# Optimization experiments

Measured on AMD Instinct MI355X. Metric: run time of the kernel, lower is better.

Reference implementation:

```python
import jax, jax.numpy as jnp
import numpy as np
from jax import lax

B, L, C_IN = 64, 2000, 4
F, K, PAD = 256, 13, 6
POOL = 4
H, DH = 8, 64
DM, NCLS = 100, 2
NOUT = L // POOL  # 500


def _rel_dist_bias():
    # RelativePosition: |clip(k - q, +-(L-1))| / (L-1), then MaxPool2d(k=POOL)
    r = jnp.arange(L)
    d = jnp.abs(jnp.clip(r[None, :] - r[:, None], -(L - 1), L - 1)).astype(jnp.float32) / (L - 1)
    d = d.reshape(NOUT, POOL, NOUT, POOL).max(axis=(1, 3))  # [NOUT, NOUT]
    return d


def setup_inputs() -> dict:
    key = jax.random.key(0)
    ks = jax.random.split(key, 8)
    s = lambda fan: 1.0 / np.sqrt(fan)
    return {
        "x": jax.random.normal(ks[0], (B, L, C_IN), jnp.float32),
        "conv_w": jax.random.normal(ks[1], (F, C_IN, K), jnp.float32) * s(C_IN * K),
        "bn_gamma": jnp.ones((F,), jnp.float32),
        "bn_beta": jnp.zeros((F,), jnp.float32),
        "Wq": jax.random.normal(ks[2], (H, F, DH), jnp.float32) * s(F),
        "bq": jnp.zeros((H, DH), jnp.float32),
        "Wk": jax.random.normal(ks[3], (H, F, DH), jnp.float32) * s(F),
        "bk": jnp.zeros((H, DH), jnp.float32),
        "Wv": jax.random.normal(ks[4], (H, F, DH), jnp.float32) * s(F),
        "bv": jnp.zeros((H, DH), jnp.float32),
        "Wm": jax.random.normal(ks[5], (H * DH, DM), jnp.float32) * s(H * DH),
        "bm": jnp.zeros((DM,), jnp.float32),
        "Wo": jax.random.normal(ks[6], (DM, NCLS), jnp.float32) * s(DM),
        "bo": jnp.zeros((NCLS,), jnp.float32),
    }


def _forward(x, conv_w, bn_gamma, bn_beta, Wq, bq, Wk, bk, Wv, bv, Wm, bm, Wo, bo):
    # CNN frontend: Conv1d (no bias) + BatchNorm (batch stats) + ReLU + MaxPool1d(4)
    xc = jnp.transpose(x, (0, 2, 1))  # [B, C_IN, L]
    y = lax.conv_general_dilated(xc, conv_w, (1,), [(PAD, PAD)],
                                 dimension_numbers=("NCH", "OIH", "NCH"))  # [B, F, L]
    mu = y.mean(axis=(0, 2), keepdims=True)
    var = y.var(axis=(0, 2), keepdims=True)
    y = bn_gamma[None, :, None] * (y - mu) * lax.rsqrt(var + 1e-5) + bn_beta[None, :, None]
    y = jax.nn.relu(y)
    y = y.reshape(B, F, NOUT, POOL).max(axis=-1)  # maxpool k=4
    h = jnp.transpose(y, (0, 2, 1))  # [B, NOUT, F]

    # Per-head Q/K/V projections (stacked over heads)
    q = jnp.einsum("bnf,hfd->bhnd", h, Wq) + bq[None, :, None, :]
    k = jnp.einsum("bnf,hfd->bhnd", h, Wk) + bk[None, :, None, :]
    v = jnp.einsum("bnf,hfd->bhnd", h, Wv) + bv[None, :, None, :]

    scores = jnp.einsum("bhnd,bhmd->bhnm", q, k) / jnp.sqrt(jnp.float32(DH))
    scores = scores - _rel_dist_bias()[None, None]  # relative-position bias
    attn = jax.nn.softmax(scores, axis=-1)
    o = jnp.einsum("bhnm,bhmd->bhnd", attn, v)  # [B, H, NOUT, DH]
    o = jnp.transpose(o, (0, 2, 1, 3)).reshape(B, NOUT, H * DH)

    m = jax.nn.relu(o @ Wm + bm)            # MultiHeadLinear + ReLU
    feat = m.sum(axis=1)                    # readout: sum over positions
    feat = (feat - feat.mean(axis=-1, keepdims=True)) / (feat.std(axis=-1, keepdims=True) + 1e-6)
    return feat @ Wo + bo                   # [B, NCLS]


def reference(x, conv_w, bn_gamma, bn_beta, Wq, bq, Wk, bk, Wv, bv, Wm, bm, Wo, bo):
    return _forward(x, conv_w, bn_gamma, bn_beta, Wq, bq, Wk, bk, Wv, bv, Wm, bm, Wo, bo)
```

## Files before the change

kernel.cpp:

```cpp
#include <hip/hip_runtime.h>
#include <stdint.h>
#include <math.h>

#define NB   64
#define LL   2000
#define CIN  4
#define NF   256
#define KW   13
#define NOUT 500
#define NH   8
#define DH   64
#define DMID 100
#define NCLS 2

#define OFF_PSUM   0
#define OFF_PSQ    16384
#define OFF_SCALE  32768
#define OFF_SHIFT  33024
#define OFF_PART   33280
#define BOFF_WT    337920ull
#define BOFF_WMT   1124352ull
#define BOFF_Q     1239040ull
#define BOFF_K     34007040ull
#define BOFF_VT    66775040ull
#define BOFF_YM    100329472ull
#define BOFF_O     BOFF_YM
#define WS_NEED    133097472ull

__device__ __forceinline__ float blo(uint32_t u) { return __uint_as_float(u << 16); }
__device__ __forceinline__ float bhi(uint32_t u) { return __uint_as_float(u & 0xFFFF0000u); }
__device__ __forceinline__ uint32_t f2bf1(float f) {
  uint32_t x = __float_as_uint(f);
  return (x + 0x7FFFu + ((x >> 16) & 1u)) >> 16;
}
__device__ __forceinline__ uint32_t pack2(float a, float b) {
  return f2bf1(a) | (f2bf1(b) << 16);
}

typedef short bf16x8 __attribute__((ext_vector_type(8)));
typedef float f32x4  __attribute__((ext_vector_type(4)));
union UB { uint4 u; bf16x8 v; };

__device__ __forceinline__ int swz(int row, int colElem) {
  return row * 128 + ((colElem * 2) ^ ((row & 7) << 4));
}

__global__ void k_prep(const float* __restrict__ Wq, const float* __restrict__ Wk,
                       const float* __restrict__ Wv, const float* __restrict__ Wm,
                       uint16_t* __restrict__ WT, uint16_t* __restrict__ WmT) {
  const int g = blockIdx.x;
  if (g < 24) {
    const int which = g >> 3, h = g & 7;
    const float* W = (which == 0 ? Wq : which == 1 ? Wk : Wv) + (size_t)h * NF * DH;
    uint16_t* dst = WT + (size_t)g * DH * NF;
    for (int idx = threadIdx.x; idx < NF * DH; idx += 256) {
      const int f = idx >> 6, d = idx & 63;
      dst[d * NF + f] = (uint16_t)f2bf1(W[idx]);
    }
  } else {
    for (int idx = threadIdx.x; idx < 112 * 512; idx += 256) {
      const int c = idx >> 9, k = idx & 511;
      WmT[idx] = (c < DMID) ? (uint16_t)f2bf1(Wm[k * DMID + c]) : (uint16_t)0;
    }
  }
}

__global__ __launch_bounds__(512) void k_conv(const float* __restrict__ x,
                                              const float* __restrict__ cw,
                                              uint16_t* __restrict__ ymaxT,
                                              float* __restrict__ psum,
                                              float* __restrict__ psq) {
  const int b = blockIdx.x;
  const int fg = blockIdx.y;
  const int tid = threadIdx.x;
  const int n = tid;
  const bool act = (n < NOUT);
  const float* xb = x + (size_t)b * (LL * CIN);

  float4 xw[16];
#pragma unroll
  for (int i = 0; i < 16; ++i) {
    const int p = 4 * n - 6 + i;
    if (act && p >= 0 && p < LL)
      xw[i] = *(const float4*)(xb + (size_t)p * CIN);
    else
      xw[i] = make_float4(0.f, 0.f, 0.f, 0.f);
  }

  __shared__ float redS[8][16];
  __shared__ float redQ[8][16];
  const int wave = tid >> 6, lane = tid & 63;
  uint32_t pw[8];
  float prev = 0.f;

  for (int fi = 0; fi < 16; ++fi) {
    const int f = fg * 16 + fi;
    const float* w = cw + (size_t)f * (CIN * KW);
    float wr[4][13];
#pragma unroll
    for (int c = 0; c < 4; ++c)
#pragma unroll
      for (int k = 0; k < 13; ++k) wr[c][k] = w[c * 13 + k];

    float a0 = 0.f, a1 = 0.f, a2 = 0.f, a3 = 0.f;
#pragma unroll
    for (int k = 0; k < 13; ++k) {
      const float4 p0 = xw[k + 0];
      const float4 p1 = xw[k + 1];
      const float4 p2 = xw[k + 2];
      const float4 p3 = xw[k + 3];
      a0 += wr[0][k] * p0.x + wr[1][k] * p0.y + wr[2][k] * p0.z + wr[3][k] * p0.w;
      a1 += wr[0][k] * p1.x + wr[1][k] * p1.y + wr[2][k] * p1.z + wr[3][k] * p1.w;
      a2 += wr[0][k] * p2.x + wr[1][k] * p2.y + wr[2][k] * p2.z + wr[3][k] * p2.w;
      a3 += wr[0][k] * p3.x + wr[1][k] * p3.y + wr[2][k] * p3.z + wr[3][k] * p3.w;
    }
    const float pm = fmaxf(fmaxf(a0, a1), fmaxf(a2, a3));
    if (fi & 1) pw[fi >> 1] = pack2(prev, pm); else prev = pm;

    float s  = act ? (a0 + a1 + a2 + a3) : 0.f;
    float q2 = act ? (a0 * a0 + a1 * a1 + a2 * a2 + a3 * a3) : 0.f;
#pragma unroll
    for (int off = 32; off >= 1; off >>= 1) {
      s  += __shfl_xor(s,  off, 64);
      q2 += __shfl_xor(q2, off, 64);
    }
    if (lane == 0) { redS[wave][fi] = s; redQ[wave][fi] = q2; }
  }
  if (act) {
    uint16_t* dst = ymaxT + ((size_t)b * NOUT + n) * NF + fg * 16;
    uint4 s0 = make_uint4(pw[0], pw[1], pw[2], pw[3]);
    uint4 s1 = make_uint4(pw[4], pw[5], pw[6], pw[7]);
    *(uint4*)dst = s0;
    *(uint4*)(dst + 8) = s1;
  }
  __syncthreads();
  if (tid < 16) {
    float s = 0.f;
#pragma unroll
    for (int wv = 0; wv < 8; ++wv) s += redS[wv][tid];
    psum[b * NF + fg * 16 + tid] = s;
  } else if (tid < 32) {
    float s = 0.f;
#pragma unroll
    for (int wv = 0; wv < 8; ++wv) s += redQ[wv][tid - 16];
    psq[b * NF + fg * 16 + (tid - 16)] = s;
  }
}

__global__ void k_stats(const float* __restrict__ psum, const float* __restrict__ psq,
                        const float* __restrict__ gamma, const float* __restrict__ beta,
                        float* __restrict__ scale, float* __restrict__ shift) {
  const int f = threadIdx.x;
  float s = 0.f, q = 0.f;
  for (int b = 0; b < NB; ++b) { s += psum[b * NF + f]; q += psq[b * NF + f]; }
  const float inv = 1.0f / (float)(NB * LL);
  const float mean = s * inv;
  const float var = q * inv - mean * mean;
  const float sc = gamma[f] * rsqrtf(var + 1e-5f);
  scale[f] = sc;
  shift[f] = beta[f] - mean * sc;
}

__global__ __launch_bounds__(256, 4) void k_qkv(const uint16_t* __restrict__ ymaxT,
     const float* __restrict__ scale, const float* __restrict__ shift,
     const uint16_t* __restrict__ WT,
     const float* __restrict__ bq, const float* __restrict__ bk, const float* __restrict__ bv,
     uint16_t* __restrict__ qb, uint16_t* __restrict__ kb, uint16_t* __restrict__ vbT) {
  const int g  = blockIdx.x;
  const int nt = blockIdx.y;
  const int b  = blockIdx.z;
  const int which = g >> 3, h = g & 7;
  const int tid = threadIdx.x;
  const int wv = tid >> 6, l = tid & 63;
  const int lg = l >> 4, lq = l & 15;
  const int n0 = nt * 64 + wv * 16;
  const uint16_t* WTg = WT + (size_t)g * DH * NF;
  const float* bias = (which == 0 ? bq : which == 1 ? bk : bv) + h * DH;

  f32x4 acc[4] = {};

  const int an = n0 + lq;
  const uint16_t* abase = ymaxT + ((size_t)b * NOUT + an) * NF;

#pragma unroll
  for (int c = 0; c < 8; ++c) {
    const int f0 = c * 32 + lg * 8;
    const uint4 ar = *(const uint4*)(abase + f0);
    const float4 s0 = *(const float4*)(scale + f0);
    const float4 s1 = *(const float4*)(scale + f0 + 4);
    const float4 h0 = *(const float4*)(shift + f0);
    const float4 h1 = *(const float4*)(shift + f0 + 4);
    UB a;
    a.u.x = pack2(fmaxf(s0.x * blo(ar.x) + h0.x, 0.f), fmaxf(s0.y * bhi(ar.x) + h0.y, 0.f));
    a.u.y = pack2(fmaxf(s0.z * blo(ar.y) + h0.z, 0.f), fmaxf(s0.w * bhi(ar.y) + h0.w, 0.f));
    a.u.z = pack2(fmaxf(s1.x * blo(ar.z) + h1.x, 0.f), fmaxf(s1.y * bhi(ar.z) + h1.y, 0.f));
    a.u.w = pack2(fmaxf(s1.z * blo(ar.w) + h1.z, 0.f), fmaxf(s1.w * bhi(ar.w) + h1.w, 0.f));
#pragma unroll
    for (int t = 0; t < 4; ++t) {
      UB bfr;
      bfr.u = *(const uint4*)(WTg + (size_t)(16 * t + lq) * NF + f0);
      acc[t] = __builtin_amdgcn_mfma_f32_16x16x32_bf16(a.v, bfr.v, acc[t], 0, 0, 0);
    }
  }

  if (which < 2) {
    uint16_t* out = (which == 0 ? qb : kb) + (size_t)(b * NH + h) * NOUT * DH;
#pragma unroll
    for (int t = 0; t < 4; ++t) {
      const int d = 16 * t + lq;
      const float bb = bias[d];
#pragma unroll
      for (int r = 0; r < 4; ++r) {
        const int nn = n0 + 4 * lg + r;
        if (nn < NOUT) out[(size_t)nn * DH + d] = (uint16_t)f2bf1(acc[t][r] + bb);
      }
    }
  } else {
    uint16_t* out = vbT + (size_t)(b * NH + h) * DH * 512;
#pragma unroll
    for (int t = 0; t < 4; ++t) {
      const int d = 16 * t + lq;
      const float bb = bias[d];
#pragma unroll
      for (int r = 0; r < 4; ++r) {
        const int nn = n0 + 4 * lg + r;
        if (nn < NOUT) out[(size_t)d * 512 + nn] = (uint16_t)f2bf1(acc[t][r] + bb);
      }
    }
  }
}

__global__ __launch_bounds__(256, 4) void k_attn(const uint16_t* __restrict__ qb,
                                                 const uint16_t* __restrict__ kb,
                                                 const uint16_t* __restrict__ vbT,
                                                 uint16_t* __restrict__ ob) {
  const int qt = blockIdx.x;
  const int h  = blockIdx.y;
  const int b  = blockIdx.z;
  const int tid = threadIdx.x;
  const int wv = tid >> 6, l = tid & 63;
  const int lg = l >> 4, lq = l & 15;

  __shared__ char smem[24576];
  char* Ks = smem;
  char* Vs = smem + 8192;
  char* Ps = smem + 16384 + wv * 2048;

  const size_t qkbase = (size_t)(b * NH + h) * NOUT * DH;
  const size_t vbase  = (size_t)(b * NH + h) * DH * 512;
  const int q0 = qt * 64 + wv * 16;

  bf16x8 qf[2];
  {
    const int qn = min(q0 + lq, NOUT - 1);
    const uint16_t* src = qb + qkbase + (size_t)qn * DH + lg * 8;
    UB t0, t1;
    t0.u = *(const uint4*)src;
    t1.u = *(const uint4*)(src + 32);
    qf[0] = t0.v; qf[1] = t1.v;
  }

  f32x4 oacc[4] = {};
  float m = -1e30f, lsum = 0.f;
  const int nq = q0 + lq;

  for (int kt = 0; kt < 8; ++kt) {
    const int kv0 = kt * 64;
    __syncthreads();
    {
      const int r = tid >> 2, cc = (tid & 3) * 16;
      const int kn = min(kv0 + r, NOUT - 1);
      const uint16_t* ksrc = kb + qkbase + (size_t)kn * DH + cc;
      uint4 ka = *(const uint4*)ksrc;
      uint4 kb4 = *(const uint4*)(ksrc + 8);
      *(uint4*)(Ks + swz(r, cc))     = ka;
      *(uint4*)(Ks + swz(r, cc + 8)) = kb4;
      const uint16_t* vsrc = vbT + vbase + (size_t)r * 512 + kv0 + cc;
      uint4 va = *(const uint4*)vsrc;
      uint4 vb4 = *(const uint4*)(vsrc + 8);
      *(uint4*)(Vs + swz(r, cc))     = va;
      *(uint4*)(Vs + swz(r, cc + 8)) = vb4;
    }
    __syncthreads();

    f32x4 sacc[4] = {};
#pragma unroll
    for (int c = 0; c < 2; ++c)
#pragma unroll
      for (int s = 0; s < 4; ++s) {
        UB kf;
        kf.u = *(const uint4*)(Ks + swz(16 * s + lq, 32 * c + 8 * lg));
        sacc[s] = __builtin_amdgcn_mfma_f32_16x16x32_bf16(kf.v, qf[c], sacc[s], 0, 0, 0);
      }

    float tmax = -1e30f;
#pragma unroll
    for (int s = 0; s < 4; ++s)
#pragma unroll
      for (int r = 0; r < 4; ++r) {
        const int nk = kv0 + 16 * s + 4 * lg + r;
        float val = sacc[s][r] * 0.125f -
                    (4.0f * fabsf((float)(nq - nk)) + 3.0f) * (1.0f / 1999.0f);
        if (nk >= NOUT) val = -1e30f;
        sacc[s][r] = val;
        tmax = fmaxf(tmax, val);
      }
    tmax = fmaxf(tmax, __shfl_xor(tmax, 16, 64));
    tmax = fmaxf(tmax, __shfl_xor(tmax, 32, 64));
    const float mnew = fmaxf(m, tmax);
    const float corr = __expf(m - mnew);
    m = mnew;
    float ls = 0.f;
#pragma unroll
    for (int s = 0; s < 4; ++s)
#pragma unroll
      for (int r = 0; r < 4; ++r) {
        const float pv = __expf(sacc[s][r] - mnew);
        sacc[s][r] = pv;
        ls += pv;
      }
    ls += __shfl_xor(ls, 16, 64);
    ls += __shfl_xor(ls, 32, 64);
    lsum = lsum * corr + ls;

#pragma unroll
    for (int s = 0; s < 4; ++s) {
      uint2 w;
      w.x = pack2(sacc[s][0], sacc[s][1]);
      w.y = pack2(sacc[s][2], sacc[s][3]);
      *(uint2*)(Ps + swz(lq, 16 * s + 4 * lg)) = w;
    }

    float cr[4];
#pragma unroll
    for (int r = 0; r < 4; ++r) cr[r] = __shfl(corr, 4 * lg + r, 64);
#pragma unroll
    for (int t = 0; t < 4; ++t)
#pragma unroll
      for (int r = 0; r < 4; ++r) oacc[t][r] *= cr[r];

#pragma unroll
    for (int c = 0; c < 2; ++c) {
      UB pf;
      pf.u = *(const uint4*)(Ps + swz(lq, 32 * c + 8 * lg));
#pragma unroll
      for (int t = 0; t < 4; ++t) {
        UB vf;
        vf.u = *(const uint4*)(Vs + swz(16 * t + lq, 32 * c + 8 * lg));
        oacc[t] = __builtin_amdgcn_mfma_f32_16x16x32_bf16(pf.v, vf.v, oacc[t], 0, 0, 0);
      }
    }
  }

  const float inv = 1.0f / lsum;
  float invr[4];
#pragma unroll
  for (int r = 0; r < 4; ++r) invr[r] = __shfl(inv, 4 * lg + r, 64);
#pragma unroll
  for (int t = 0; t < 4; ++t) {
    const int d = 16 * t + lq;
#pragma unroll
    for (int r = 0; r < 4; ++r) {
      const int nn = q0 + 4 * lg + r;
      if (nn < NOUT)
        ob[((size_t)b * NOUT + nn) * (NH * DH) + h * DH + d] =
            (uint16_t)f2bf1(oacc[t][r] * invr[r]);
    }
  }
}

__global__ __launch_bounds__(256, 4) void k_mhl(const uint16_t* __restrict__ ob,
                                                const uint16_t* __restrict__ WmT,
                                                const float* __restrict__ bm,
                                                float* __restrict__ part) {
  const int nt = blockIdx.x;
  const int b  = blockIdx.y;
  const int tid = threadIdx.x;
  const int wv = tid >> 6, l = tid & 63;
  const int lg = l >> 4, lq = l & 15;
  const int n0 = nt * 64 + wv * 16;

  __shared__ float lfeat[4][112];

  f32x4 acc[7] = {};
  const int an = min(n0 + lq, NOUT - 1);
  const uint16_t* abase = ob + ((size_t)b * NOUT + an) * (NH * DH);

  for (int kc = 0; kc < 16; ++kc) {
    const int k0 = kc * 32 + lg * 8;
    UB a;
    a.u = *(const uint4*)(abase + k0);
#pragma unroll
    for (int t = 0; t < 7; ++t) {
      UB bfr;
      bfr.u = *(const uint4*)(WmT + (size_t)(16 * t + lq) * 512 + k0);
      acc[t] = __builtin_amdgcn_mfma_f32_16x16x32_bf16(a.v, bfr.v, acc[t], 0, 0, 0);
    }
  }

#pragma unroll
  for (int t = 0; t < 7; ++t) {
    const int c = 16 * t + lq;
    const float bb = (c < DMID) ? bm[c] : 0.f;
    float s = 0.f;
#pragma unroll
    for (int r = 0; r < 4; ++r) {
      const int nn = n0 + 4 * lg + r;
      if (nn < NOUT) s += fmaxf(acc[t][r] + bb, 0.f);
    }
    s += __shfl_xor(s, 16, 64);
    s += __shfl_xor(s, 32, 64);
    if (lg == 0) lfeat[wv][c] = s;
  }
  __syncthreads();
  if (tid < DMID)
    part[((size_t)b * 8 + nt) * DMID + tid] =
        lfeat[0][tid] + lfeat[1][tid] + lfeat[2][tid] + lfeat[3][tid];
}

__global__ void k_head(const float* __restrict__ part, const float* __restrict__ Wo,
                       const float* __restrict__ bo, float* __restrict__ out) {
  const int b = threadIdx.x;
  float s1 = 0.f;
  for (int c = 0; c < DMID; ++c) {
    float v = 0.f;
    for (int t = 0; t < 8; ++t) v += part[((size_t)b * 8 + t) * DMID + c];
    s1 += v;
  }
  const float mean = s1 / (float)DMID;
  float s2 = 0.f;
  for (int c = 0; c < DMID; ++c) {
    float v = 0.f;
    for (int t = 0; t < 8; ++t) v += part[((size_t)b * 8 + t) * DMID + c];
    const float d = v - mean;
    s2 += d * d;
  }
  const float inv = 1.0f / (sqrtf(s2 / (float)DMID) + 1e-6f);
  float o0 = bo[0], o1 = bo[1];
  for (int c = 0; c < DMID; ++c) {
    float v = 0.f;
    for (int t = 0; t < 8; ++t) v += part[((size_t)b * 8 + t) * DMID + c];
    const float nz = (v - mean) * inv;
    o0 += nz * Wo[c * 2 + 0];
    o1 += nz * Wo[c * 2 + 1];
  }
  out[b * 2 + 0] = o0;
  out[b * 2 + 1] = o1;
}

extern "C" void kernel_launch(void* const* d_in, const int* in_sizes, int n_in,
                              void* d_out, int out_size, void* d_ws, size_t ws_size,
                              hipStream_t stream) {
  (void)in_sizes; (void)n_in; (void)out_size;
  const float* x     = (const float*)d_in[0];
  const float* cw    = (const float*)d_in[1];
  const float* gamma = (const float*)d_in[2];
  const float* beta  = (const float*)d_in[3];
  const float* Wq    = (const float*)d_in[4];
  const float* bq    = (const float*)d_in[5];
  const float* Wk    = (const float*)d_in[6];
  const float* bk    = (const float*)d_in[7];
  const float* Wv    = (const float*)d_in[8];
  const float* bv    = (const float*)d_in[9];
  const float* Wm    = (const float*)d_in[10];
  const float* bm    = (const float*)d_in[11];
  const float* Wo    = (const float*)d_in[12];
  const float* bo    = (const float*)d_in[13];
  float* out = (float*)d_out;

  if (ws_size < WS_NEED) return;

  float* wsf = (float*)d_ws;
  float* psum  = wsf + OFF_PSUM;
  float* psq   = wsf + OFF_PSQ;
  float* scale = wsf + OFF_SCALE;
  float* shift = wsf + OFF_SHIFT;
  float* partf = wsf + OFF_PART;
  uint16_t* WTb   = (uint16_t*)((char*)d_ws + BOFF_WT);
  uint16_t* WmT   = (uint16_t*)((char*)d_ws + BOFF_WMT);
  uint16_t* qbuf  = (uint16_t*)((char*)d_ws + BOFF_Q);
  uint16_t* kbuf  = (uint16_t*)((char*)d_ws + BOFF_K);
  uint16_t* vbT   = (uint16_t*)((char*)d_ws + BOFF_VT);
  uint16_t* ymaxT = (uint16_t*)((char*)d_ws + BOFF_YM);
  uint16_t* obuf  = (uint16_t*)((char*)d_ws + BOFF_O);

  k_prep <<<25, 256, 0, stream>>>(Wq, Wk, Wv, Wm, WTb, WmT);
  k_conv <<<dim3(NB, 16), 512, 0, stream>>>(x, cw, ymaxT, psum, psq);
  k_stats<<<1, NF, 0, stream>>>(psum, psq, gamma, beta, scale, shift);
  k_qkv  <<<dim3(24, 8, NB), 256, 0, stream>>>(ymaxT, scale, shift, WTb, bq, bk, bv,
                                               qbuf, kbuf, vbT);
  k_attn <<<dim3(8, NH, NB), 256, 0, stream>>>(qbuf, kbuf, vbT, obuf);
  k_mhl  <<<dim3(8, NB), 256, 0, stream>>>(obuf, WmT, bm, partf);
  k_head <<<1, NB, 0, stream>>>(partf, Wo, bo, out);
}
```

Before: 690.3 us.

## Stage normalized activations in LDS and reuse across heads in QKV projection

The QKV kernel now launches one block per (Q/K/V, 64-row tile, batch) instead of one per head. Each block applies the BN affine and ReLU to its 64x256 activation tile once and stores it in swizzled LDS. Each wave then computes two heads from that shared tile, and the MFMA operand order is arranged so outputs are written as packed 4-element vectors, transposed for V. This removes the repeated global reads and normalization of the activation tile for every head and widens the stores, but cuts the grid 8x (1536 blocks) and raises register use per wave.

```diff
diff --git a/kernel.cpp b/kernel.cpp
--- a/kernel.cpp
+++ b/kernel.cpp
@@ -44,6 +44,9 @@
 __device__ __forceinline__ int swz(int row, int colElem) {
   return row * 128 + ((colElem * 2) ^ ((row & 7) << 4));
 }
+__device__ __forceinline__ int addrA(int row, int f) {
+  return row * 512 + (((f >> 3) ^ (row & 7)) << 4) + ((f & 7) * 2);
+}
 
 __global__ void k_prep(const float* __restrict__ Wq, const float* __restrict__ Wk,
                        const float* __restrict__ Wv, const float* __restrict__ Wm,
@@ -166,65 +169,109 @@
      const uint16_t* __restrict__ WT,
      const float* __restrict__ bq, const float* __restrict__ bk, const float* __restrict__ bv,
      uint16_t* __restrict__ qb, uint16_t* __restrict__ kb, uint16_t* __restrict__ vbT) {
-  const int g  = blockIdx.x;
+  const int which = blockIdx.x;
   const int nt = blockIdx.y;
   const int b  = blockIdx.z;
-  const int which = g >> 3, h = g & 7;
   const int tid = threadIdx.x;
   const int wv = tid >> 6, l = tid & 63;
   const int lg = l >> 4, lq = l & 15;
-  const int n0 = nt * 64 + wv * 16;
-  const uint16_t* WTg = WT + (size_t)g * DH * NF;
-  const float* bias = (which == 0 ? bq : which == 1 ? bk : bv) + h * DH;
-
-  f32x4 acc[4] = {};
-
-  const int an = n0 + lq;
-  const uint16_t* abase = ymaxT + ((size_t)b * NOUT + an) * NF;
-
-#pragma unroll
-  for (int c = 0; c < 8; ++c) {
-    const int f0 = c * 32 + lg * 8;
-    const uint4 ar = *(const uint4*)(abase + f0);
+  const int n0 = nt * 64;
+
+  __shared__ char smem[32768 + 2048];
+  char* ldsA = smem;
+  float* biasLds = (float*)(smem + 32768);
+
+  {
+    const int col16 = tid & 31;
+    const int f0 = col16 * 8;
     const float4 s0 = *(const float4*)(scale + f0);
     const float4 s1 = *(const float4*)(scale + f0 + 4);
     const float4 h0 = *(const float4*)(shift + f0);
     const float4 h1 = *(const float4*)(shift + f0 + 4);
-    UB a;
-    a.u.x = pack2(fmaxf(s0.x * blo(ar.x) + h0.x, 0.f), fmaxf(s0.y * bhi(ar.x) + h0.y, 0.f));
-    a.u.y = pack2(fmaxf(s0.z * blo(ar.y) + h0.z, 0.f), fmaxf(s0.w * bhi(ar.y) + h0.w, 0.f));
-    a.u.z = pack2(fmaxf(s1.x * blo(ar.z) + h1.x, 0.f), fmaxf(s1.y * bhi(ar.z) + h1.y, 0.f));
-    a.u.w = pack2(fmaxf(s1.z * blo(ar.w) + h1.z, 0.f), fmaxf(s1.w * bhi(ar.w) + h1.w, 0.f));
-#pragma unroll
-    for (int t = 0; t < 4; ++t) {
-      UB bfr;
-      bfr.u = *(const uint4*)(WTg + (size_t)(16 * t + lq) * NF + f0);
-      acc[t] = __builtin_amdgcn_mfma_f32_16x16x32_bf16(a.v, bfr.v, acc[t], 0, 0, 0);
-    }
-  }
-
-  if (which < 2) {
-    uint16_t* out = (which == 0 ? qb : kb) + (size_t)(b * NH + h) * NOUT * DH;
-#pragma unroll
-    for (int t = 0; t < 4; ++t) {
-      const int d = 16 * t + lq;
-      const float bb = bias[d];
-#pragma unroll
-      for (int r = 0; r < 4; ++r) {
-        const int nn = n0 + 4 * lg + r;
-        if (nn < NOUT) out[(size_t)nn * DH + d] = (uint16_t)f2bf1(acc[t][r] + bb);
-      }
-    }
-  } else {
-    uint16_t* out = vbT + (size_t)(b * NH + h) * DH * 512;
-#pragma unroll
-    for (int t = 0; t < 4; ++t) {
-      const int d = 16 * t + lq;
-      const float bb = bias[d];
-#pragma unroll
-      for (int r = 0; r < 4; ++r) {
-        const int nn = n0 + 4 * lg + r;
-        if (nn < NOUT) out[(size_t)d * 512 + nn] = (uint16_t)f2bf1(acc[t][r] + bb);
+#pragma unroll
+    for (int p = 0; p < 8; ++p) {
+      const int row = p * 8 + (tid >> 5);
+      const int n = min(n0 + row, NOUT - 1);
+      const uint4 u = *(const uint4*)(ymaxT + ((size_t)b * NOUT + n) * NF + f0);
+      uint4 o;
+      o.x = pack2(fmaxf(s0.x * blo(u.x) + h0.x, 0.f), fmaxf(s0.y * bhi(u.x) + h0.y, 0.f));
+      o.y = pack2(fmaxf(s0.z * blo(u.y) + h0.z, 0.f), fmaxf(s0.w * bhi(u.y) + h0.w, 0.f));
+      o.z = pack2(fmaxf(s1.x * blo(u.z) + h1.x, 0.f), fmaxf(s1.y * bhi(u.z) + h1.y, 0.f));
+      o.w = pack2(fmaxf(s1.z * blo(u.w) + h1.z, 0.f), fmaxf(s1.w * bhi(u.w) + h1.w, 0.f));
+      *(uint4*)(ldsA + addrA(row, f0)) = o;
+    }
+    const float* biasW = (which == 0 ? bq : which == 1 ? bk : bv);
+    biasLds[tid] = biasW[tid];
+    biasLds[tid + 256] = biasW[tid + 256];
+  }
+  __syncthreads();
+
+  for (int hi = 0; hi < 2; ++hi) {
+    const int h = wv + hi * 4;
+    const uint16_t* WTg = WT + (size_t)(which * 8 + h) * DH * NF;
+
+    f32x4 acc[4][4] = {};
+#pragma unroll
+    for (int c = 0; c < 8; ++c) {
+      const int f0 = c * 32 + lg * 8;
+      UB wf[4], hf[4];
+#pragma unroll
+      for (int dt = 0; dt < 4; ++dt)
+        wf[dt].u = *(const uint4*)(WTg + (size_t)(16 * dt + lq) * NF + f0);
+#pragma unroll
+      for (int s = 0; s < 4; ++s)
+        hf[s].u = *(const uint4*)(ldsA + addrA(16 * s + lq, f0));
+      if (which < 2) {
+#pragma unroll
+        for (int dt = 0; dt < 4; ++dt)
+#pragma unroll
+          for (int s = 0; s < 4; ++s)
+            acc[dt][s] = __builtin_amdgcn_mfma_f32_16x16x32_bf16(wf[dt].v, hf[s].v, acc[dt][s], 0, 0, 0);
+      } else {
+#pragma unroll
+        for (int s = 0; s < 4; ++s)
+#pragma unroll
+          for (int dt = 0; dt < 4; ++dt)
+            acc[s][dt] = __builtin_amdgcn_mfma_f32_16x16x32_bf16(hf[s].v, wf[dt].v, acc[s][dt], 0, 0, 0);
+      }
+    }
+
+    if (which < 2) {
+      uint16_t* out = (which == 0 ? qb : kb) + (size_t)(b * NH + h) * NOUT * DH;
+#pragma unroll
+      for (int dt = 0; dt < 4; ++dt) {
+        const int d0 = 16 * dt + 4 * lg;
+        const float bb0 = biasLds[h * DH + d0 + 0];
+        const float bb1 = biasLds[h * DH + d0 + 1];
+        const float bb2 = biasLds[h * DH + d0 + 2];
+        const float bb3 = biasLds[h * DH + d0 + 3];
+#pragma unroll
+        for (int s = 0; s < 4; ++s) {
+          const int n = n0 + 16 * s + lq;
+          if (n < NOUT) {
+            uint2 w;
+            w.x = pack2(acc[dt][s][0] + bb0, acc[dt][s][1] + bb1);
+            w.y = pack2(acc[dt][s][2] + bb2, acc[dt][s][3] + bb3);
+            *(uint2*)(out + (size_t)n * DH + d0) = w;
+          }
+        }
+      }
+    } else {
+      uint16_t* out = vbT + (size_t)(b * NH + h) * DH * 512;
+#pragma unroll
+      for (int s = 0; s < 4; ++s) {
+        const int nb4 = n0 + 16 * s + 4 * lg;
+        if (nb4 < NOUT) {
+#pragma unroll
+          for (int dt = 0; dt < 4; ++dt) {
+            const int d = 16 * dt + lq;
+            const float bb = biasLds[h * DH + d];
+            uint2 w;
+            w.x = pack2(acc[s][dt][0] + bb, acc[s][dt][1] + bb);
+            w.y = pack2(acc[s][dt][2] + bb, acc[s][dt][3] + bb);
+            *(uint2*)(out + (size_t)d * 512 + nb4) = w;
+          }
+        }
       }
     }
   }
@@ -487,8 +534,8 @@
   k_prep <<<25, 256, 0, stream>>>(Wq, Wk, Wv, Wm, WTb, WmT);
   k_conv <<<dim3(NB, 16), 512, 0, stream>>>(x, cw, ymaxT, psum, psq);
   k_stats<<<1, NF, 0, stream>>>(psum, psq, gamma, beta, scale, shift);
-  k_qkv  <<<dim3(24, 8, NB), 256, 0, stream>>>(ymaxT, scale, shift, WTb, bq, bk, bv,
-                                               qbuf, kbuf, vbT);
+  k_qkv  <<<dim3(3, 8, NB), 256, 0, stream>>>(ymaxT, scale, shift, WTb, bq, bk, bv,
+                                              qbuf, kbuf, vbT);
   k_attn <<<dim3(8, NH, NB), 256, 0, stream>>>(qbuf, kbuf, vbT, obuf);
   k_mhl  <<<dim3(8, NB), 256, 0, stream>>>(obuf, WmT, bm, partf);
   k_head <<<1, NB, 0, stream>>>(partf, Wo, bo, out);
```

Result: slower. 767.0 us (+11.1%).
